# Kernel optimization log

Measured on AMD Instinct MI355X. Metric: run time of the kernel, lower is better.

## Reference

```python
import jax, jax.numpy as jnp
import numpy as np

B, T, H = 2048, 200, 128
H1, H2 = 80, 40
NEG = -1e9  # stand-in for -inf so masked-row grads stay finite


def setup_inputs() -> dict:
    key = jax.random.key(0)
    ks = jax.random.split(key, 8)
    query = jax.random.normal(ks[0], (B, H), dtype=jnp.float32)
    keys = jax.random.normal(ks[1], (B, T, H), dtype=jnp.float32)
    keys_length = jax.random.randint(ks[2], (B,), 1, T + 1, dtype=jnp.int32)
    W1 = jax.random.normal(ks[3], (4 * H, H1), dtype=jnp.float32) * (1.0 / np.sqrt(4 * H))
    b1 = jnp.zeros((H1,), dtype=jnp.float32)
    W2 = jax.random.normal(ks[4], (H1, H2), dtype=jnp.float32) * (1.0 / np.sqrt(H1))
    b2 = jnp.zeros((H2,), dtype=jnp.float32)
    Wf = jax.random.normal(ks[5], (H2, 1), dtype=jnp.float32) * (1.0 / np.sqrt(H2))
    bf = jnp.zeros((1,), dtype=jnp.float32)
    return {"query": query, "keys": keys, "keys_length": keys_length,
            "W1": W1, "b1": b1, "W2": W2, "b2": b2, "Wf": Wf, "bf": bf}


def reference(query, keys, keys_length, W1, b1, W2, b2, Wf, bf):
    # query: [B,H] -> broadcast over T; build DIN feature concat [B,T,4H]
    q = jnp.broadcast_to(query[:, None, :], keys.shape)
    din = jnp.concatenate([q, keys, q - keys, q * keys], axis=-1)  # [B,T,4H]
    h = jax.nn.relu(jnp.einsum('btf,fk->btk', din, W1) + b1)       # [B,T,H1]
    h = jax.nn.relu(jnp.einsum('btk,km->btm', h, W2) + b2)         # [B,T,H2]
    scores = (jnp.einsum('btm,mo->bto', h, Wf) + bf)[..., 0]       # [B,T]
    scores = scores / jnp.sqrt(jnp.float32(keys.shape[-1]))
    mask = jnp.arange(keys.shape[1]) < keys_length[:, None]        # [B,T]
    scores = jnp.where(mask, scores, NEG)
    attn = jax.nn.softmax(scores, axis=1)                          # [B,T]
    out = jnp.einsum('bt,bth->bh', attn, keys)                     # [B,H]
    return out
```

## Files before the change

### kernel.cpp

```cpp
#include <hip/hip_runtime.h>
#include <stdint.h>


#define B_SZ   2048
#define T_SZ   200
#define H_SZ   128
#define H1_SZ  80
#define H2_SZ  40
#define TPAD   208
#define NMT    13
#define NEG_VAL (-1e9f)
#define SCALE_V 0.08838834764831845f

#define WS_BCF 0
#define WS_DDF 40960
#define WS_W2S 81920
#define WS_ACF 91136

typedef __attribute__((ext_vector_type(8))) short short8v;
typedef __attribute__((ext_vector_type(4))) short short4v;
typedef __attribute__((ext_vector_type(4))) float f32x4;

static __device__ __forceinline__ short f2bf(float f) {
    union { float f; uint32_t u; } x; x.f = f;
    uint32_t r = x.u + 0x7fffu + ((x.u >> 16) & 1u);
    return (short)(r >> 16);
}
static __device__ __forceinline__ float bf2f(short s) {
    union { uint32_t u; float f; } x; x.u = ((uint32_t)(uint16_t)s) << 16;
    return x.f;
}

__global__ void din_prep(const float* __restrict__ W1, const float* __restrict__ W2,
                         float* __restrict__ bcf, float* __restrict__ ddf,
                         short* __restrict__ w2s, float* __restrict__ acf)
{
    const int blk = blockIdx.x, tid = threadIdx.x;
    if (blk < 20) {
        const int fidx = blk, kt = fidx / 5, nt = fidx % 5;
        #pragma unroll
        for (int e = tid; e < 512; e += 256) {
            int l = e >> 3, j = e & 7;
            int k = kt * 32 + (l >> 4) * 8 + j;
            int n = nt * 16 + (l & 15);
            bcf[fidx * 512 + e] = W1[(128 + k) * 80 + n] - W1[(256 + k) * 80 + n];
            ddf[fidx * 512 + e] = W1[(384 + k) * 80 + n];
        }
    } else if (blk < 29) {
        const int fidx = blk - 20, kt = fidx / 3, nt = fidx % 3;
        #pragma unroll
        for (int e = tid; e < 512; e += 256) {
            int l = e >> 3, j = e & 7;
            int k = kt * 32 + (l >> 4) * 8 + j;
            int n = nt * 16 + (l & 15);
            float wv = (k < H1_SZ && n < H2_SZ) ? W2[k * H2_SZ + n] : 0.f;
            w2s[fidx * 512 + e] = f2bf(wv);
        }
    } else {
        const int base = (blk - 29) * 1024;
        #pragma unroll
        for (int i = 0; i < 4; ++i) {
            int e = base + i * 256 + tid;
            int n = e >> 7, k = e & 127;
            acf[e] = W1[k * 80 + n] + W1[(256 + k) * 80 + n];
        }
    }
}

__global__ __launch_bounds__(256, 2)
void din_attn_kernel(const float* __restrict__ query, const float* __restrict__ keys,
                     const int* __restrict__ klen_arr, const float* __restrict__ b1,
                     const float* __restrict__ b2, const float* __restrict__ Wf,
                     const float* __restrict__ bfp, const float* __restrict__ bcf,
                     const float* __restrict__ ddf, const short* __restrict__ w2s,
                     const float* __restrict__ acf, float* __restrict__ out)
{
    __shared__ __align__(16) short sK[TPAD * H_SZ];
    __shared__ __align__(16) short sH1[4][16 * 96];
    __shared__ float sS[TPAD];
    __shared__ float sP[TPAD];
    __shared__ float sBias1[H1_SZ];
    __shared__ float sB2[48];
    __shared__ float sWf[48];
    __shared__ float sRed[4], sRedL[4];
    __shared__ float sOutF[4][H_SZ];

    const int tid  = threadIdx.x;
    const int b    = blockIdx.x;
    const int w    = tid >> 6;
    const int lane = tid & 63;
    const int lo   = lane & 15;
    const int hi   = lane >> 4;
    const int klen = klen_arr[b];
    const float bf0 = bfp[0];
    const float* qg = query + (size_t)b * H_SZ;

    if (tid >= 128 && tid < 176) { int n = tid - 128; sB2[n] = (n < H2_SZ) ? b2[n] : 0.f; }
    if (tid >= 176 && tid < 224) { int n = tid - 176; sWf[n] = (n < H2_SZ) ? Wf[n] : 0.f; }

    const float* kb = keys + (size_t)b * T_SZ * H_SZ;
    #pragma unroll
    for (int i = 0; i < 25; ++i) {
        int idx = tid + i * 256;
        int row = idx >> 5, c4 = idx & 31;
        const float4 v = *(const float4*)(kb + row * H_SZ + c4 * 4);
        short4v s;
        s[0] = f2bf(v.x); s[1] = f2bf(v.y); s[2] = f2bf(v.z); s[3] = f2bf(v.w);
        int sidx = ((row << 7) + (c4 << 2)) ^ ((row & 7) << 3);
        *(short4v*)&sK[sidx] = s;
    }
    {
        int row = 200 + (tid >> 5), c4 = tid & 31;
        int sidx = ((row << 7) + (c4 << 2)) ^ ((row & 7) << 3);
        short4v z = {0, 0, 0, 0};
        *(short4v*)&sK[sidx] = z;
    }

    short8v b1f[4][5];
    #pragma unroll
    for (int kt = 0; kt < 4; ++kt) {
        const float4 q0 = *(const float4*)(qg + kt * 32 + hi * 8);
        const float4 q1 = *(const float4*)(qg + kt * 32 + hi * 8 + 4);
        const float qv[8] = {q0.x, q0.y, q0.z, q0.w, q1.x, q1.y, q1.z, q1.w};
        #pragma unroll
        for (int nt = 0; nt < 5; ++nt) {
            const int base = ((kt * 5 + nt) * 64 + lane) * 8;
            const float4 c0 = *(const float4*)(bcf + base);
            const float4 c1 = *(const float4*)(bcf + base + 4);
            const float4 d0 = *(const float4*)(ddf + base);
            const float4 d1 = *(const float4*)(ddf + base + 4);
            short8v v;
            v[0] = f2bf(c0.x + qv[0] * d0.x);
            v[1] = f2bf(c0.y + qv[1] * d0.y);
            v[2] = f2bf(c0.z + qv[2] * d0.z);
            v[3] = f2bf(c0.w + qv[3] * d0.w);
            v[4] = f2bf(c1.x + qv[4] * d1.x);
            v[5] = f2bf(c1.y + qv[5] * d1.y);
            v[6] = f2bf(c1.z + qv[6] * d1.z);
            v[7] = f2bf(c1.w + qv[7] * d1.w);
            b1f[kt][nt] = v;
        }
    }
    short8v b2f[3][3];
    #pragma unroll
    for (int kt = 0; kt < 3; ++kt)
        #pragma unroll
        for (int nt = 0; nt < 3; ++nt)
            b2f[kt][nt] = *(const short8v*)(w2s + ((kt * 3 + nt) * 64 + lane) * 8);

    if (tid < H1_SZ) {
        float acc = b1[tid];
        const float* ar = acf + tid * H_SZ;
        #pragma unroll
        for (int i = 0; i < 32; ++i) {
            const float4 wv = *(const float4*)(ar + i * 4);
            const float4 q4 = *(const float4*)(qg + i * 4);
            acc += wv.x * q4.x + wv.y * q4.y + wv.z * q4.z + wv.w * q4.w;
        }
        sBias1[tid] = acc;
    }
    __syncthreads();

    for (int mt = w; mt < NMT; mt += 4) {
        const int t0 = mt << 4;
        f32x4 acc1[5];
        #pragma unroll
        for (int nt = 0; nt < 5; ++nt) acc1[nt] = (f32x4){0.f, 0.f, 0.f, 0.f};
        #pragma unroll
        for (int kt = 0; kt < 4; ++kt) {
            int row  = t0 + lo;
            int sidx = ((row << 7) + (kt << 5) + (hi << 3)) ^ ((row & 7) << 3);
            short8v a = *(short8v*)&sK[sidx];
            #pragma unroll
            for (int nt = 0; nt < 5; ++nt)
                acc1[nt] = __builtin_amdgcn_mfma_f32_16x16x32_bf16(a, b1f[kt][nt], acc1[nt], 0, 0, 0);
        }
        short* h1p = &sH1[w][0];
        #pragma unroll
        for (int nt = 0; nt < 5; ++nt) {
            int n = nt * 16 + lo;
            float bias = sBias1[n];
            #pragma unroll
            for (int r = 0; r < 4; ++r) {
                int rl = hi * 4 + r;
                float v = fmaxf(acc1[nt][r] + bias, 0.f);
                h1p[rl * 96 + n] = f2bf(v);
            }
        }
        {
            int n = 80 + lo;
            #pragma unroll
            for (int r = 0; r < 4; ++r) h1p[(hi * 4 + r) * 96 + n] = 0;
        }
        asm volatile("s_waitcnt lgkmcnt(0)" ::: "memory");

        f32x4 acc2[3];
        #pragma unroll
        for (int nt = 0; nt < 3; ++nt) acc2[nt] = (f32x4){0.f, 0.f, 0.f, 0.f};
        #pragma unroll
        for (int kt = 0; kt < 3; ++kt) {
            short8v a2 = *(short8v*)&h1p[lo * 96 + kt * 32 + hi * 8];
            #pragma unroll
            for (int nt = 0; nt < 3; ++nt)
                acc2[nt] = __builtin_amdgcn_mfma_f32_16x16x32_bf16(a2, b2f[kt][nt], acc2[nt], 0, 0, 0);
        }
        float sc[4] = {0.f, 0.f, 0.f, 0.f};
        #pragma unroll
        for (int nt = 0; nt < 3; ++nt) {
            int n = nt * 16 + lo;
            float bb = sB2[n], wfv = sWf[n];
            #pragma unroll
            for (int r = 0; r < 4; ++r)
                sc[r] += fmaxf(acc2[nt][r] + bb, 0.f) * wfv;
        }
        #pragma unroll
        for (int m = 1; m <= 8; m <<= 1)
            #pragma unroll
            for (int r = 0; r < 4; ++r)
                sc[r] += __shfl_xor(sc[r], m, 16);
        if (lo == 0) {
            #pragma unroll
            for (int r = 0; r < 4; ++r) {
                int t = t0 + hi * 4 + r;
                sS[t] = (t < klen) ? (sc[r] + bf0) * SCALE_V : NEG_VAL;
            }
        }
    }
    __syncthreads();

    float v = (tid < TPAD) ? sS[tid] : -3.0e38f;
    #pragma unroll
    for (int m = 32; m >= 1; m >>= 1) v = fmaxf(v, __shfl_xor(v, m, 64));
    if (lane == 0) sRed[w] = v;
    __syncthreads();
    const float mx = fmaxf(fmaxf(sRed[0], sRed[1]), fmaxf(sRed[2], sRed[3]));
    float pv = 0.f;
    if (tid < TPAD) { pv = __expf(sS[tid] - mx); sP[tid] = pv; }
    #pragma unroll
    for (int m = 32; m >= 1; m >>= 1) pv += __shfl_xor(pv, m, 64);
    if (lane == 0) sRedL[w] = pv;
    __syncthreads();
    const float inv_l = 1.0f / (sRedL[0] + sRedL[1] + sRedL[2] + sRedL[3]);

    {
        const int hp = (tid & 63) * 2;
        const int c  = tid >> 6;
        float a0 = 0.f, a1 = 0.f;
        #pragma unroll 4
        for (int i = 0; i < 52; ++i) {
            int t = c * 52 + i;
            int sidx = ((t << 7) + hp) ^ ((t & 7) << 3);
            uint32_t pk = *(const uint32_t*)&sK[sidx];
            float p = sP[t];
            a0 += p * bf2f((short)(pk & 0xffff));
            a1 += p * bf2f((short)(pk >> 16));
        }
        sOutF[c][hp]     = a0;
        sOutF[c][hp + 1] = a1;
    }
    __syncthreads();
    if (tid < H_SZ)
        out[(size_t)b * H_SZ + tid] =
            (sOutF[0][tid] + sOutF[1][tid] + sOutF[2][tid] + sOutF[3][tid]) * inv_l;
}

extern "C" void kernel_launch(void* const* d_in, const int* in_sizes, int n_in,
                              void* d_out, int out_size, void* d_ws, size_t ws_size,
                              hipStream_t stream) {
    const float* query = (const float*)d_in[0];
    const float* keys  = (const float*)d_in[1];
    const int*   klen  = (const int*)d_in[2];
    const float* W1    = (const float*)d_in[3];
    const float* b1    = (const float*)d_in[4];
    const float* W2    = (const float*)d_in[5];
    const float* b2    = (const float*)d_in[6];
    const float* Wf    = (const float*)d_in[7];
    const float* bfp   = (const float*)d_in[8];
    float* outp = (float*)d_out;
    (void)in_sizes; (void)n_in; (void)out_size; (void)ws_size;

    char* ws = (char*)d_ws;
    float* bcf = (float*)(ws + WS_BCF);
    float* ddf = (float*)(ws + WS_DDF);
    short* w2s = (short*)(ws + WS_W2S);
    float* acf = (float*)(ws + WS_ACF);

    din_prep<<<39, 256, 0, stream>>>(W1, W2, bcf, ddf, w2s, acf);
    din_attn_kernel<<<B_SZ, 256, 0, stream>>>(query, keys, klen, b1, b2, Wf, bfp,
                                              bcf, ddf, w2s, acf, outp);
}
```

Measured before the change: 435.8 us.

## Split each batch row across two blocks with flash-style softmax merge kernel

Each batch element's 200 timesteps are now split across two workgroups of 100 rows. Each half writes a partial output plus its max and sum to workspace, and a new merge kernel combines the halves with log-sum-exp rescaling. Per-block shared memory drops, which should allow more resident blocks and better latency hiding. The query-dependent layer-1 weight fragments now sit in shared memory instead of registers, easing register pressure at the cost of extra LDS reads, and the H1 row stride is padded to 104. In exchange there is an extra kernel launch, a workspace round trip, and duplicated per-block setup (bias and weight-fragment computation) for every half.

```diff
diff --git a/kernel.cpp b/kernel.cpp
--- a/kernel.cpp
+++ b/kernel.cpp
@@ -7,8 +7,10 @@
 #define H_SZ   128
 #define H1_SZ  80
 #define H2_SZ  40
-#define TPAD   208
-#define NMT    13
+#define THALF  100
+#define TPAD_H 112
+#define NMT_H  7
+#define H1LD   104
 #define NEG_VAL (-1e9f)
 #define SCALE_V 0.08838834764831845f
 
@@ -16,6 +18,8 @@
 #define WS_DDF 40960
 #define WS_W2S 81920
 #define WS_ACF 91136
+#define WS_O   132096
+#define WS_ML  2229248
 
 typedef __attribute__((ext_vector_type(8))) short short8v;
 typedef __attribute__((ext_vector_type(4))) short short4v;
@@ -73,12 +77,15 @@
                      const float* __restrict__ b2, const float* __restrict__ Wf,
                      const float* __restrict__ bfp, const float* __restrict__ bcf,
                      const float* __restrict__ ddf, const short* __restrict__ w2s,
-                     const float* __restrict__ acf, float* __restrict__ out)
+                     const float* __restrict__ acf, float* __restrict__ wsO,
+                     float* __restrict__ wsML)
 {
-    __shared__ __align__(16) short sK[TPAD * H_SZ];
-    __shared__ __align__(16) short sH1[4][16 * 96];
-    __shared__ float sS[TPAD];
-    __shared__ float sP[TPAD];
+    __shared__ __align__(16) short sK[TPAD_H * H_SZ];
+    __shared__ __align__(16) short sB1F[20 * 512];
+    __shared__ __align__(16) short sH1[4][16 * H1LD];
+    __shared__ __align__(16) float sQ[H_SZ];
+    __shared__ float sS[TPAD_H];
+    __shared__ float sP[TPAD_H];
     __shared__ float sBias1[H1_SZ];
     __shared__ float sB2[48];
     __shared__ float sWf[48];
@@ -86,7 +93,8 @@
     __shared__ float sOutF[4][H_SZ];
 
     const int tid  = threadIdx.x;
-    const int b    = blockIdx.x;
+    const int b    = blockIdx.x >> 1;
+    const int half = blockIdx.x & 1;
     const int w    = tid >> 6;
     const int lane = tid & 63;
     const int lo   = lane & 15;
@@ -95,50 +103,31 @@
     const float bf0 = bfp[0];
     const float* qg = query + (size_t)b * H_SZ;
 
+    if (tid < H_SZ) sQ[tid] = qg[tid];
     if (tid >= 128 && tid < 176) { int n = tid - 128; sB2[n] = (n < H2_SZ) ? b2[n] : 0.f; }
     if (tid >= 176 && tid < 224) { int n = tid - 176; sWf[n] = (n < H2_SZ) ? Wf[n] : 0.f; }
 
-    const float* kb = keys + (size_t)b * T_SZ * H_SZ;
-    #pragma unroll
-    for (int i = 0; i < 25; ++i) {
+    const float* kb = keys + ((size_t)b * T_SZ + half * THALF) * H_SZ;
+    #pragma unroll
+    for (int i = 0; i < 13; ++i) {
         int idx = tid + i * 256;
-        int row = idx >> 5, c4 = idx & 31;
-        const float4 v = *(const float4*)(kb + row * H_SZ + c4 * 4);
-        short4v s;
-        s[0] = f2bf(v.x); s[1] = f2bf(v.y); s[2] = f2bf(v.z); s[3] = f2bf(v.w);
-        int sidx = ((row << 7) + (c4 << 2)) ^ ((row & 7) << 3);
-        *(short4v*)&sK[sidx] = s;
-    }
-    {
-        int row = 200 + (tid >> 5), c4 = tid & 31;
-        int sidx = ((row << 7) + (c4 << 2)) ^ ((row & 7) << 3);
-        short4v z = {0, 0, 0, 0};
-        *(short4v*)&sK[sidx] = z;
-    }
-
-    short8v b1f[4][5];
-    #pragma unroll
-    for (int kt = 0; kt < 4; ++kt) {
-        const float4 q0 = *(const float4*)(qg + kt * 32 + hi * 8);
-        const float4 q1 = *(const float4*)(qg + kt * 32 + hi * 8 + 4);
-        const float qv[8] = {q0.x, q0.y, q0.z, q0.w, q1.x, q1.y, q1.z, q1.w};
-        #pragma unroll
-        for (int nt = 0; nt < 5; ++nt) {
-            const int base = ((kt * 5 + nt) * 64 + lane) * 8;
-            const float4 c0 = *(const float4*)(bcf + base);
-            const float4 c1 = *(const float4*)(bcf + base + 4);
-            const float4 d0 = *(const float4*)(ddf + base);
-            const float4 d1 = *(const float4*)(ddf + base + 4);
-            short8v v;
-            v[0] = f2bf(c0.x + qv[0] * d0.x);
-            v[1] = f2bf(c0.y + qv[1] * d0.y);
-            v[2] = f2bf(c0.z + qv[2] * d0.z);
-            v[3] = f2bf(c0.w + qv[3] * d0.w);
-            v[4] = f2bf(c1.x + qv[4] * d1.x);
-            v[5] = f2bf(c1.y + qv[5] * d1.y);
-            v[6] = f2bf(c1.z + qv[6] * d1.z);
-            v[7] = f2bf(c1.w + qv[7] * d1.w);
-            b1f[kt][nt] = v;
+        if (idx < 3200) {
+            int row = idx >> 5, c4 = idx & 31;
+            const float4 v = *(const float4*)(kb + row * H_SZ + c4 * 4);
+            short4v s;
+            s[0] = f2bf(v.x); s[1] = f2bf(v.y); s[2] = f2bf(v.z); s[3] = f2bf(v.w);
+            int sidx = ((row << 7) + (c4 << 2)) ^ ((row & 7) << 3);
+            *(short4v*)&sK[sidx] = s;
+        }
+    }
+    #pragma unroll
+    for (int i = 0; i < 2; ++i) {
+        int idx = tid + i * 256;
+        if (idx < 384) {
+            int row = THALF + (idx >> 5), c4 = idx & 31;
+            int sidx = ((row << 7) + (c4 << 2)) ^ ((row & 7) << 3);
+            short4v z = {0, 0, 0, 0};
+            *(short4v*)&sK[sidx] = z;
         }
     }
     short8v b2f[3][3];
@@ -147,21 +136,39 @@
         #pragma unroll
         for (int nt = 0; nt < 3; ++nt)
             b2f[kt][nt] = *(const short8v*)(w2s + ((kt * 3 + nt) * 64 + lane) * 8);
-
+    __syncthreads();
+
+    #pragma unroll
+    for (int i = 0; i < 10; ++i) {
+        int g = tid + i * 256;
+        int fidx = g >> 7;
+        int kt = fidx / 5;
+        int l = (g >> 1) & 63, j0 = (g & 1) * 4;
+        int k0 = kt * 32 + ((l >> 4) << 3) + j0;
+        const float4 c = *(const float4*)(bcf + g * 4);
+        const float4 d = *(const float4*)(ddf + g * 4);
+        const float4 q4 = *(const float4*)(sQ + k0);
+        short4v s;
+        s[0] = f2bf(c.x + q4.x * d.x);
+        s[1] = f2bf(c.y + q4.y * d.y);
+        s[2] = f2bf(c.z + q4.z * d.z);
+        s[3] = f2bf(c.w + q4.w * d.w);
+        *(short4v*)&sB1F[g * 4] = s;
+    }
     if (tid < H1_SZ) {
         float acc = b1[tid];
         const float* ar = acf + tid * H_SZ;
         #pragma unroll
         for (int i = 0; i < 32; ++i) {
             const float4 wv = *(const float4*)(ar + i * 4);
-            const float4 q4 = *(const float4*)(qg + i * 4);
+            const float4 q4 = *(const float4*)(sQ + i * 4);
             acc += wv.x * q4.x + wv.y * q4.y + wv.z * q4.z + wv.w * q4.w;
         }
         sBias1[tid] = acc;
     }
     __syncthreads();
 
-    for (int mt = w; mt < NMT; mt += 4) {
+    for (int mt = w; mt < NMT_H; mt += 4) {
         const int t0 = mt << 4;
         f32x4 acc1[5];
         #pragma unroll
@@ -172,8 +179,10 @@
             int sidx = ((row << 7) + (kt << 5) + (hi << 3)) ^ ((row & 7) << 3);
             short8v a = *(short8v*)&sK[sidx];
             #pragma unroll
-            for (int nt = 0; nt < 5; ++nt)
-                acc1[nt] = __builtin_amdgcn_mfma_f32_16x16x32_bf16(a, b1f[kt][nt], acc1[nt], 0, 0, 0);
+            for (int nt = 0; nt < 5; ++nt) {
+                short8v bfr = *(short8v*)&sB1F[((kt * 5 + nt) * 64 + lane) * 8];
+                acc1[nt] = __builtin_amdgcn_mfma_f32_16x16x32_bf16(a, bfr, acc1[nt], 0, 0, 0);
+            }
         }
         short* h1p = &sH1[w][0];
         #pragma unroll
@@ -184,13 +193,13 @@
             for (int r = 0; r < 4; ++r) {
                 int rl = hi * 4 + r;
                 float v = fmaxf(acc1[nt][r] + bias, 0.f);
-                h1p[rl * 96 + n] = f2bf(v);
+                h1p[rl * H1LD + n] = f2bf(v);
             }
         }
         {
             int n = 80 + lo;
             #pragma unroll
-            for (int r = 0; r < 4; ++r) h1p[(hi * 4 + r) * 96 + n] = 0;
+            for (int r = 0; r < 4; ++r) h1p[(hi * 4 + r) * H1LD + n] = 0;
         }
         asm volatile("s_waitcnt lgkmcnt(0)" ::: "memory");
 
@@ -199,7 +208,7 @@
         for (int nt = 0; nt < 3; ++nt) acc2[nt] = (f32x4){0.f, 0.f, 0.f, 0.f};
         #pragma unroll
         for (int kt = 0; kt < 3; ++kt) {
-            short8v a2 = *(short8v*)&h1p[lo * 96 + kt * 32 + hi * 8];
+            short8v a2 = *(short8v*)&h1p[lo * H1LD + kt * 32 + hi * 8];
             #pragma unroll
             for (int nt = 0; nt < 3; ++nt)
                 acc2[nt] = __builtin_amdgcn_mfma_f32_16x16x32_bf16(a2, b2f[kt][nt], acc2[nt], 0, 0, 0);
@@ -221,34 +230,39 @@
         if (lo == 0) {
             #pragma unroll
             for (int r = 0; r < 4; ++r) {
-                int t = t0 + hi * 4 + r;
-                sS[t] = (t < klen) ? (sc[r] + bf0) * SCALE_V : NEG_VAL;
+                int tl = t0 + hi * 4 + r;
+                int tg = half * THALF + tl;
+                bool valid = (tl < THALF) && (tg < klen);
+                sS[tl] = valid ? (sc[r] + bf0) * SCALE_V : NEG_VAL;
             }
         }
     }
     __syncthreads();
 
-    float v = (tid < TPAD) ? sS[tid] : -3.0e38f;
+    float v = (tid < TPAD_H) ? sS[tid] : -3.0e38f;
     #pragma unroll
     for (int m = 32; m >= 1; m >>= 1) v = fmaxf(v, __shfl_xor(v, m, 64));
     if (lane == 0) sRed[w] = v;
     __syncthreads();
     const float mx = fmaxf(fmaxf(sRed[0], sRed[1]), fmaxf(sRed[2], sRed[3]));
     float pv = 0.f;
-    if (tid < TPAD) { pv = __expf(sS[tid] - mx); sP[tid] = pv; }
+    if (tid < TPAD_H) { pv = __expf(sS[tid] - mx); sP[tid] = pv; }
     #pragma unroll
     for (int m = 32; m >= 1; m >>= 1) pv += __shfl_xor(pv, m, 64);
     if (lane == 0) sRedL[w] = pv;
     __syncthreads();
-    const float inv_l = 1.0f / (sRedL[0] + sRedL[1] + sRedL[2] + sRedL[3]);
+    if (tid == 0) {
+        wsML[b * 4 + half * 2 + 0] = mx;
+        wsML[b * 4 + half * 2 + 1] = sRedL[0] + sRedL[1] + sRedL[2] + sRedL[3];
+    }
 
     {
         const int hp = (tid & 63) * 2;
         const int c  = tid >> 6;
         float a0 = 0.f, a1 = 0.f;
         #pragma unroll 4
-        for (int i = 0; i < 52; ++i) {
-            int t = c * 52 + i;
+        for (int i = 0; i < 28; ++i) {
+            int t = c * 28 + i;
             int sidx = ((t << 7) + hp) ^ ((t & 7) << 3);
             uint32_t pk = *(const uint32_t*)&sK[sidx];
             float p = sP[t];
@@ -260,8 +274,23 @@
     }
     __syncthreads();
     if (tid < H_SZ)
-        out[(size_t)b * H_SZ + tid] =
-            (sOutF[0][tid] + sOutF[1][tid] + sOutF[2][tid] + sOutF[3][tid]) * inv_l;
+        wsO[((size_t)b * 2 + half) * H_SZ + tid] =
+            sOutF[0][tid] + sOutF[1][tid] + sOutF[2][tid] + sOutF[3][tid];
+}
+
+__global__ void din_merge(const float* __restrict__ wsO, const float* __restrict__ wsML,
+                          float* __restrict__ out)
+{
+    int g = blockIdx.x * 256 + threadIdx.x;
+    int b = g >> 7, h = g & 127;
+    float m0 = wsML[b * 4 + 0], l0 = wsML[b * 4 + 1];
+    float m1 = wsML[b * 4 + 2], l1 = wsML[b * 4 + 3];
+    float M  = fmaxf(m0, m1);
+    float w0 = __expf(m0 - M), w1 = __expf(m1 - M);
+    float denom = w0 * l0 + w1 * l1;
+    float o0 = wsO[((size_t)b * 2 + 0) * 128 + h];
+    float o1 = wsO[((size_t)b * 2 + 1) * 128 + h];
+    out[g] = (w0 * o0 + w1 * o1) / denom;
 }
 
 extern "C" void kernel_launch(void* const* d_in, const int* in_sizes, int n_in,
@@ -280,12 +309,15 @@
     (void)in_sizes; (void)n_in; (void)out_size; (void)ws_size;
 
     char* ws = (char*)d_ws;
-    float* bcf = (float*)(ws + WS_BCF);
-    float* ddf = (float*)(ws + WS_DDF);
-    short* w2s = (short*)(ws + WS_W2S);
-    float* acf = (float*)(ws + WS_ACF);
+    float* bcf  = (float*)(ws + WS_BCF);
+    float* ddf  = (float*)(ws + WS_DDF);
+    short* w2s  = (short*)(ws + WS_W2S);
+    float* acf  = (float*)(ws + WS_ACF);
+    float* wsO  = (float*)(ws + WS_O);
+    float* wsML = (float*)(ws + WS_ML);
 
     din_prep<<<39, 256, 0, stream>>>(W1, W2, bcf, ddf, w2s, acf);
-    din_attn_kernel<<<B_SZ, 256, 0, stream>>>(query, keys, klen, b1, b2, Wf, bfp,
-                                              bcf, ddf, w2s, acf, outp);
-}
+    din_attn_kernel<<<B_SZ * 2, 256, 0, stream>>>(query, keys, klen, b1, b2, Wf, bfp,
+                                                  bcf, ddf, w2s, acf, wsO, wsML);
+    din_merge<<<(B_SZ * H_SZ) / 256, 256, 0, stream>>>(wsO, wsML, outp);
+}
```

Measured after the change: 356.5 us. -18.2%, faster.
